# Optimization experiments

Measured on AMD Instinct MI355X. Metric: run time of the kernel, lower is better.

Reference implementation:

```python
import jax, jax.numpy as jnp
import numpy as np

EPS = 1e-8
MIN_VAL = -1e7  # min_val for masked_max padding


def _cos(v1, v2, axis=-1):
    # torch.F.cosine_similarity: dot / (max(||v1||,eps) * max(||v2||,eps))
    n1 = jnp.maximum(jnp.linalg.norm(v1, axis=axis), EPS)
    n2 = jnp.maximum(jnp.linalg.norm(v2, axis=axis), EPS)
    return jnp.sum(v1 * v2, axis=axis) / (n1 * n2)


def _mpm(v1, v2, w):
    # v1: (B,S,H), v2: (B,S,H) or (B,1,H), w: (P,H)
    mv_one = _cos(v1, v2)[..., None]                 # (B,S,1)
    v1w = w[None, None] * v1[:, :, None, :]          # (B,S,P,H)
    v2w = w[None, None] * v2[:, :, None, :]          # (B,S or 1,P,H)
    mv_many = _cos(v1w, v2w)                          # (B,S,P)
    return mv_one, mv_many


def _mpm_pairwise(v1, v2, w):
    # v1: (B,S1,H), v2: (B,S2,H), w: (P,H) -> (B,S1,S2,P)
    v1w = w[None, :, None, :] * v1[:, None]          # (B,P,S1,H)
    v2w = w[None, :, None, :] * v2[:, None]          # (B,P,S2,H)
    n1 = jnp.linalg.norm(v1w, axis=3)[..., None]     # (B,P,S1,1)
    n2 = jnp.linalg.norm(v2w, axis=3)[..., None]     # (B,P,S2,1)
    mul = jnp.einsum('bpih,bpjh->bpij', v1w, v2w)    # (B,P,S1,S2)
    norm = jnp.maximum(n1 * jnp.swapaxes(n2, 2, 3), EPS)
    return jnp.transpose(mul / norm, (0, 2, 3, 1))


def _masked_max(v, m, axis, keepdims=False):
    return jnp.max(v + (1.0 - m) * MIN_VAL, axis=axis, keepdims=keepdims)


def _masked_mean(v, m, axis, keepdims=False):
    s = jnp.sum(v, axis=axis, keepdims=keepdims)
    c = jnp.sum(m, axis=axis, keepdims=keepdims)
    return s / jnp.maximum(c, EPS)


def _bimpm(context_p, mask_p, context_h, mask_h, w_full, w_maxpool, w_att, w_maxatt):
    mp = mask_p.astype(context_p.dtype)              # (B,S1)
    mh = mask_h.astype(context_h.dtype)              # (B,S2)
    len_p = jnp.sum(mask_p, axis=1)
    len_h = jnp.sum(mask_h, axis=1)
    cp = context_p * mp[..., None]
    ch = context_h * mh[..., None]

    # pairwise cosine similarity (B,S1,S2)
    cos = _cos(cp[:, :, None, :], ch[:, None, :, :])
    cos_max_p = _masked_max(cos, mh[:, None, :], 2, True)
    cos_mean_p = _masked_mean(cos, mh[:, None, :], 2, True)
    cosT = jnp.swapaxes(cos, 1, 2)
    cos_max_h = _masked_max(cosT, mp[:, None, :], 2, True)
    cos_mean_h = _masked_mean(cosT, mp[:, None, :], 2, True)
    mv_p = [cos_max_p, cos_mean_p]
    mv_h = [cos_max_h, cos_mean_h]

    # full match (is_forward=True -> use last valid token)
    B, _, H = cp.shape
    idx_p = jnp.maximum(len_p - 1, 0)[:, None, None]
    idx_h = jnp.maximum(len_h - 1, 0)[:, None, None]
    last_p = jnp.take_along_axis(cp, jnp.broadcast_to(idx_p, (B, 1, H)), axis=1)
    last_h = jnp.take_along_axis(ch, jnp.broadcast_to(idx_h, (B, 1, H)), axis=1)
    o, m = _mpm(cp, last_h, w_full); mv_p += [o, m]
    o, m = _mpm(ch, last_p, w_full); mv_h += [o, m]

    # maxpool match over pairwise multi-perspective cosines (B,S1,S2,P)
    pw = _mpm_pairwise(cp, ch, w_maxpool)
    mv_p += [_masked_max(pw, mh[:, None, :, None], 2),
             _masked_mean(pw, mh[:, None, :, None], 2)]
    pwT = jnp.transpose(pw, (0, 2, 1, 3))
    mv_h += [_masked_max(pwT, mp[:, None, :, None], 2),
             _masked_mean(pwT, mp[:, None, :, None], 2)]

    # attentive match (mean-weighted by cosine attention)
    att = cos
    att_mean_h = jnp.einsum('bij,bjh->bih', att, ch) / jnp.maximum(
        jnp.sum(att, axis=2, keepdims=True), EPS)        # (B,S1,H)
    att_mean_p = jnp.einsum('bij,bih->bjh', att, cp) / jnp.maximum(
        jnp.swapaxes(jnp.sum(att, axis=1, keepdims=True), 1, 2), EPS)  # (B,S2,H)
    o, m = _mpm(cp, att_mean_h, w_att); mv_p += [o, m]
    o, m = _mpm(ch, att_mean_p, w_att); mv_h += [o, m]

    # max attentive match
    att_h_full = ch[:, None, :, :] * att[..., None]      # (B,S1,S2,H)
    att_max_h = _masked_max(att_h_full, mh[:, None, :, None], 2)  # (B,S1,H)
    att_p_full = cp[:, :, None, :] * att[..., None]      # (B,S1,S2,H)
    att_max_p = _masked_max(att_p_full, mp[:, :, None, None], 1)  # (B,S2,H)
    o, m = _mpm(cp, att_max_h, w_maxatt); mv_p += [o, m]
    o, m = _mpm(ch, att_max_p, w_maxatt); mv_h += [o, m]

    # (2, B, S, output_dim=105)
    return jnp.stack([jnp.concatenate(mv_p, axis=-1),
                      jnp.concatenate(mv_h, axis=-1)], axis=0)


def setup_inputs() -> dict:
    B, S1, S2, H, P = 8, 256, 256, 100, 20
    key = jax.random.key(0)
    ks = jax.random.split(key, 8)
    context_p = jax.random.normal(ks[0], (B, S1, H), jnp.float32)
    context_h = jax.random.normal(ks[1], (B, S2, H), jnp.float32)
    len_p = jax.random.randint(ks[2], (B,), S1 // 2, S1 + 1)
    len_h = jax.random.randint(ks[3], (B,), S2 // 2, S2 + 1)
    mask_p = (jnp.arange(S1)[None, :] < len_p[:, None]).astype(jnp.int32)
    mask_h = (jnp.arange(S2)[None, :] < len_h[:, None]).astype(jnp.int32)
    # four matching weights (share_weight_between_directions=True), torch.rand -> U[0,1)
    w_full = jax.random.uniform(ks[4], (P, H), jnp.float32)
    w_maxpool = jax.random.uniform(ks[5], (P, H), jnp.float32)
    w_att = jax.random.uniform(ks[6], (P, H), jnp.float32)
    w_maxatt = jax.random.uniform(ks[7], (P, H), jnp.float32)
    return {"context_p": context_p, "mask_p": mask_p, "context_h": context_h,
            "mask_h": mask_h, "w_full": w_full, "w_maxpool": w_maxpool,
            "w_att": w_att, "w_maxatt": w_maxatt}


def reference(context_p, mask_p, context_h, mask_h, w_full, w_maxpool, w_att, w_maxatt):
    return _bimpm(context_p, mask_p, context_h, mask_h, w_full, w_maxpool, w_att, w_maxatt)
```

## Files before the change

kernel.cpp:

```cpp
#include <hip/hip_runtime.h>

#define Bq 8
#define Sq 256
#define Hq 100
#define Pq 20
#define PPq 21
#define Fq 105
#define EPSq 1e-8f
#define NEGB -1e30f
#define IMG (128 * 136)

typedef short bf16x8 __attribute__((ext_vector_type(8)));
typedef float f32x4 __attribute__((ext_vector_type(4)));

__device__ __forceinline__ unsigned fkey(float f) {
    unsigned b = __float_as_uint(f);
    return (b & 0x80000000u) ? ~b : (b | 0x80000000u);
}
__device__ __forceinline__ float funkey(unsigned k) {
    return __uint_as_float((k & 0x80000000u) ? (k ^ 0x80000000u) : ~k);
}
__device__ __forceinline__ unsigned short bf16rn(float f) {
    unsigned u = __float_as_uint(f);
    unsigned r = u + 0x7FFFu + ((u >> 16) & 1u);
    return (unsigned short)(r >> 16);
}
__device__ __forceinline__ unsigned mulpack(unsigned pair, float w0, float w1) {
    float f0 = __uint_as_float(pair << 16);
    float f1 = __uint_as_float(pair & 0xFFFF0000u);
    f0 *= w0; f1 *= w1;
    return ((unsigned)bf16rn(f0)) | (((unsigned)bf16rn(f1)) << 16);
}

__global__ __launch_bounds__(256) void k_prep(
    const float* __restrict__ ctx_p, const int* __restrict__ mask_p,
    const float* __restrict__ ctx_h, const int* __restrict__ mask_h,
    const float* __restrict__ w_mp,
    float* __restrict__ vm, float* __restrict__ vmT,
    float* __restrict__ mf, float* __restrict__ wn,
    unsigned short* __restrict__ a16,
    float* __restrict__ lens, int* __restrict__ lasts,
    unsigned* __restrict__ statinit) {
    __shared__ float tileT[Hq * 257];
    __shared__ float w2T[Hq * 20];
    __shared__ float smf[256];
    __shared__ int ired[256];
    int side = blockIdx.x >> 3;
    int b = blockIdx.x & 7;
    int t = threadIdx.x;

    for (int idx = blockIdx.x * 256 + t; idx < 4 * Bq * PPq * Sq; idx += 16 * 256)
        statinit[idx] = 0u;

    const float* ctx = side ? ctx_h : ctx_p;
    const int* mask = side ? mask_h : mask_p;
    int mi = mask[b * Sq + t];
    smf[t] = (float)mi;
    ired[t] = mi;
    for (int idx = t; idx < Pq * Hq; idx += 256) {
        int p = idx / Hq, h = idx - p * Hq;
        float w = w_mp[idx];
        w2T[h * 20 + p] = w * w;
    }
    __syncthreads();
    for (int o = 128; o; o >>= 1) {
        if (t < o) ired[t] += ired[t + o];
        __syncthreads();
    }
    if (t == 0) {
        int l = ired[0];
        lens[side * Bq + b] = (float)l;
        lasts[side * Bq + b] = l > 0 ? l - 1 : 0;
    }

    unsigned short* abase = a16 + (size_t)(side * Bq + b) * 2 * IMG;
    {
        ushort4 z = {0, 0, 0, 0};
        for (int idx = t; idx < 2304; idx += 256) {
            int half = idx >= 1152;
            int rr = idx - half * 1152;
            int r = rr / 9, c = rr - r * 9;
            *(ushort4*)(abase + half * IMG + r * 136 + 100 + c * 4) = z;
        }
    }

    const float4* src = (const float4*)(ctx + (size_t)b * Sq * Hq);
    float4* vmo = (float4*)(vm + ((size_t)side * Bq + b) * Sq * Hq);
#pragma unroll
    for (int q = 0; q < 25; q++) {
        int F = t + 256 * q;
        int s = F / 25;
        int c = F - s * 25;
        float m = smf[s];
        float4 v4 = src[F];
        v4.x *= m; v4.y *= m; v4.z *= m; v4.w *= m;
        vmo[F] = v4;
        int h0 = c * 4;
        tileT[(h0 + 0) * 257 + s] = v4.x;
        tileT[(h0 + 1) * 257 + s] = v4.y;
        tileT[(h0 + 2) * 257 + s] = v4.z;
        tileT[(h0 + 3) * 257 + s] = v4.w;
        ushort4 o;
        o.x = bf16rn(v4.x); o.y = bf16rn(v4.y); o.z = bf16rn(v4.z); o.w = bf16rn(v4.w);
        *(ushort4*)(abase + (s >> 7) * IMG + (s & 127) * 136 + c * 4) = o;
    }
    __syncthreads();

    int s = t;
    float acc[PPq];
#pragma unroll
    for (int p = 0; p < PPq; p++) acc[p] = 0.f;
    float* vmTo = vmT + ((size_t)side * Bq + b) * Hq * Sq;
#pragma unroll 4
    for (int h = 0; h < Hq; h++) {
        float v = tileT[h * 257 + s];
        vmTo[h * Sq + s] = v;
        float e = v * v;
        acc[Pq] += e;
        const float4* wrow = (const float4*)(w2T + h * 20);
#pragma unroll
        for (int pq = 0; pq < 5; pq++) {
            float4 w4 = wrow[pq];
            acc[pq * 4 + 0] += w4.x * e;
            acc[pq * 4 + 1] += w4.y * e;
            acc[pq * 4 + 2] += w4.z * e;
            acc[pq * 4 + 3] += w4.w * e;
        }
    }
    float* wout = wn + ((size_t)side * Bq + b) * PPq * Sq;
#pragma unroll
    for (int p = 0; p < PPq; p++)
        wout[p * Sq + s] = 1.f / fmaxf(sqrtf(acc[p]), EPSq);
    mf[(size_t)side * Bq * Sq + b * Sq + s] = smf[s];
}

__global__ __launch_bounds__(256) void k_pw(
    const unsigned short* __restrict__ a16,
    const float* __restrict__ vmT,
    const float* __restrict__ wn, const float* __restrict__ mf,
    const float* __restrict__ w_mp, const float* __restrict__ lens,
    float* __restrict__ out, float* __restrict__ cosm, float* __restrict__ cosT,
    unsigned* __restrict__ rowmax, float* __restrict__ rowsum,
    unsigned* __restrict__ colmax, float* __restrict__ colsum) {
    __shared__ unsigned short As[IMG];
    __shared__ unsigned short Bs[IMG];
    __shared__ float w2s[144];
    int blk = blockIdx.x;
    int t = threadIdx.x;

    if (blk >= 64) {
        int mblk = blk - 64;
        int b = mblk / 80;
        int rem = mblk - b * 80;
        int p = rem >> 2;
        int ih = (rem >> 1) & 1, jh = rem & 1;
        int i0 = ih * 128, j0 = jh * 128;

        if (t < 144) {
            float w = (t < Hq) ? w_mp[p * Hq + t] : 0.f;
            w2s[t] = w * w;
        }
        __syncthreads();

        {
            const uint4* sa = (const uint4*)(a16 + (size_t)(b * 2 + ih) * IMG);
            uint4* dA = (uint4*)As;
#pragma unroll
            for (int q = 0; q < 9; q++) {
                int idx = t + 256 * q;
                if (idx < 2176) dA[idx] = sa[idx];
            }
        }
        {
            const uint4* sb = (const uint4*)(a16 + (size_t)((Bq + b) * 2 + jh) * IMG);
            uint4* dB = (uint4*)Bs;
#pragma unroll
            for (int q = 0; q < 9; q++) {
                int idx = t + 256 * q;
                if (idx < 2176) {
                    int cc = idx - (idx / 17) * 17;
                    int hb = cc * 8;
                    uint4 ch = sb[idx];
                    float4 wA = *(const float4*)(w2s + hb);
                    float4 wB = *(const float4*)(w2s + hb + 4);
                    uint4 o;
                    o.x = mulpack(ch.x, wA.x, wA.y);
                    o.y = mulpack(ch.y, wA.z, wA.w);
                    o.z = mulpack(ch.z, wB.x, wB.y);
                    o.w = mulpack(ch.w, wB.z, wB.w);
                    dB[idx] = o;
                }
            }
        }
        __syncthreads();

        int lane = t & 63;
        int wv = t >> 6;
        int wr = wv & 1, wc = wv >> 1;
        int lm = lane & 15, lq = lane >> 4;

        f32x4 acc[4][4];
#pragma unroll
        for (int tm = 0; tm < 4; tm++)
#pragma unroll
            for (int tn = 0; tn < 4; tn++) acc[tm][tn] = 0.f;

#pragma unroll
        for (int ks = 0; ks < 4; ks++) {
            bf16x8 af[4], bfr[4];
#pragma unroll
            for (int tm = 0; tm < 4; tm++)
                af[tm] = *(const bf16x8*)&As[(wr * 64 + tm * 16 + lm) * 136 + ks * 32 + lq * 8];
#pragma unroll
            for (int tn = 0; tn < 4; tn++)
                bfr[tn] = *(const bf16x8*)&Bs[(wc * 64 + tn * 16 + lm) * 136 + ks * 32 + lq * 8];
#pragma unroll
            for (int tm = 0; tm < 4; tm++)
#pragma unroll
                for (int tn = 0; tn < 4; tn++)
                    acc[tm][tn] = __builtin_amdgcn_mfma_f32_16x16x32_bf16(af[tm], bfr[tn], acc[tm][tn], 0, 0, 0);
        }

        const float* wn0 = wn + ((size_t)b * PPq + p) * Sq;
        const float* wn1 = wn + ((size_t)(Bq + b) * PPq + p) * Sq;
        const float* mfp = mf + b * Sq;
        const float* mfh = mf + (size_t)Bq * Sq + b * Sq;
        size_t base = ((size_t)b * PPq + p) * Sq;
        float rn2v[4], mzh[4];
#pragma unroll
        for (int tn = 0; tn < 4; tn++) {
            int jj = j0 + wc * 64 + tn * 16 + lm;
            rn2v[tn] = wn1[jj];
            mzh[tn] = mfh[jj] > 0.5f ? 0.f : NEGB;
        }
        float cmax[4] = {NEGB, NEGB, NEGB, NEGB};
        float csum[4] = {0.f, 0.f, 0.f, 0.f};
#pragma unroll
        for (int tm = 0; tm < 4; tm++) {
            int ibase = i0 + wr * 64 + tm * 16 + lq * 4;
            float rn1v[4], mzp[4];
#pragma unroll
            for (int r2 = 0; r2 < 4; r2++) {
                rn1v[r2] = wn0[ibase + r2];
                mzp[r2] = mfp[ibase + r2] > 0.5f ? 0.f : NEGB;
            }
            float rmax[4] = {NEGB, NEGB, NEGB, NEGB};
            float rsum[4] = {0.f, 0.f, 0.f, 0.f};
#pragma unroll
            for (int tn = 0; tn < 4; tn++)
#pragma unroll
                for (int r2 = 0; r2 < 4; r2++) {
                    float v = acc[tm][tn][r2] * rn1v[r2] * rn2v[tn];
                    rmax[r2] = fmaxf(rmax[r2], v + mzh[tn]);
                    rsum[r2] += v;
                    cmax[tn] = fmaxf(cmax[tn], v + mzp[r2]);
                    csum[tn] += v;
                }
#pragma unroll
            for (int r2 = 0; r2 < 4; r2++)
#pragma unroll
                for (int o = 1; o < 16; o <<= 1) {
                    rmax[r2] = fmaxf(rmax[r2], __shfl_xor(rmax[r2], o, 64));
                    rsum[r2] += __shfl_xor(rsum[r2], o, 64);
                }
            if (lm == 0) {
#pragma unroll
                for (int r2 = 0; r2 < 4; r2++) {
                    atomicMax(rowmax + base + ibase + r2, fkey(rmax[r2]));
                    atomicAdd(rowsum + base + ibase + r2, rsum[r2]);
                }
            }
        }
#pragma unroll
        for (int tn = 0; tn < 4; tn++) {
#pragma unroll
            for (int o = 16; o < 64; o <<= 1) {
                cmax[tn] = fmaxf(cmax[tn], __shfl_xor(cmax[tn], o, 64));
                csum[tn] += __shfl_xor(csum[tn], o, 64);
            }
        }
        if (lq == 0) {
#pragma unroll
            for (int tn = 0; tn < 4; tn++) {
                int jj = j0 + wc * 64 + tn * 16 + lm;
                atomicMax(colmax + base + jj, fkey(cmax[tn]));
                atomicAdd(colsum + base + jj, csum[tn]);
            }
        }
        return;
    }

    float (*cbmax)[Sq] = (float (*)[Sq])As;
    float (*cbsum)[Sq] = (float (*)[Sq])(As + 8192);
    int b = blk >> 3, it = blk & 7;
    int lane = t & 63;
    int wid = __builtin_amdgcn_readfirstlane(t >> 6);
    int i0 = it * 32 + wid * 8;

    const float* abase2 = vmT + (size_t)b * Hq * Sq;
    const float* bbase2 = vmT + (size_t)(Bq + b) * Hq * Sq;

    float4 acc[8];
#pragma unroll
    for (int k = 0; k < 8; k++) acc[k] = make_float4(0.f, 0.f, 0.f, 0.f);

#pragma unroll 4
    for (int h = 0; h < Hq; h++) {
        float4 bq = ((const float4*)(bbase2 + h * Sq))[lane];
        const float4* ap = (const float4*)(abase2 + h * Sq + i0);
        float4 a0 = ap[0], a1 = ap[1];
        float av[8] = {a0.x, a0.y, a0.z, a0.w, a1.x, a1.y, a1.z, a1.w};
#pragma unroll
        for (int k = 0; k < 8; k++) {
            acc[k].x += av[k] * bq.x; acc[k].y += av[k] * bq.y;
            acc[k].z += av[k] * bq.z; acc[k].w += av[k] * bq.w;
        }
    }

    const float* wn0 = wn + ((size_t)b * PPq + Pq) * Sq;
    const float* wn1 = wn + ((size_t)(Bq + b) * PPq + Pq) * Sq;
    float4 rn2 = ((const float4*)wn1)[lane];
    float4 mh4 = ((const float4*)(mf + (size_t)Bq * Sq + b * Sq))[lane];
    float invLh = 1.f / fmaxf(lens[Bq + b], EPSq);

    float cmax[4] = {NEGB, NEGB, NEGB, NEGB};
    float csum[4] = {0.f, 0.f, 0.f, 0.f};
#pragma unroll
    for (int k = 0; k < 8; k++) {
        float r1 = wn0[i0 + k];
        float4 v;
        v.x = acc[k].x * r1 * rn2.x;
        v.y = acc[k].y * r1 * rn2.y;
        v.z = acc[k].z * r1 * rn2.z;
        v.w = acc[k].w * r1 * rn2.w;
        float m0 = mh4.x > 0.5f ? v.x : NEGB;
        float m1 = mh4.y > 0.5f ? v.y : NEGB;
        float m2 = mh4.z > 0.5f ? v.z : NEGB;
        float m3 = mh4.w > 0.5f ? v.w : NEGB;
        float rmax = fmaxf(fmaxf(m0, m1), fmaxf(m2, m3));
        float rs = v.x + v.y + v.z + v.w;
        for (int o = 32; o; o >>= 1) {
            rmax = fmaxf(rmax, __shfl_xor(rmax, o, 64));
            rs += __shfl_xor(rs, o, 64);
        }
        if (lane == 0) {
            float* orow = out + ((size_t)(b * Sq + i0 + k)) * Fq;
            orow[0] = rmax;
            orow[1] = rs * invLh;
        }
        float mi = mf[b * Sq + i0 + k];
        if (mi > 0.5f) {
            cmax[0] = fmaxf(cmax[0], v.x); cmax[1] = fmaxf(cmax[1], v.y);
            cmax[2] = fmaxf(cmax[2], v.z); cmax[3] = fmaxf(cmax[3], v.w);
        }
        csum[0] += v.x; csum[1] += v.y; csum[2] += v.z; csum[3] += v.w;
        ((float4*)(cosm + (size_t)(b * Sq + i0 + k) * Sq))[lane] = v;
        int jb = 4 * lane;
        cosT[((size_t)b * Sq + jb + 0) * Sq + i0 + k] = v.x;
        cosT[((size_t)b * Sq + jb + 1) * Sq + i0 + k] = v.y;
        cosT[((size_t)b * Sq + jb + 2) * Sq + i0 + k] = v.z;
        cosT[((size_t)b * Sq + jb + 3) * Sq + i0 + k] = v.w;
    }
    ((float4*)&cbmax[wid][0])[lane] = make_float4(cmax[0], cmax[1], cmax[2], cmax[3]);
    ((float4*)&cbsum[wid][0])[lane] = make_float4(csum[0], csum[1], csum[2], csum[3]);
    __syncthreads();
    {
        int j = t;
        float mx = fmaxf(fmaxf(cbmax[0][j], cbmax[1][j]), fmaxf(cbmax[2][j], cbmax[3][j]));
        float sm = cbsum[0][j] + cbsum[1][j] + cbsum[2][j] + cbsum[3][j];
        size_t cidx = ((size_t)b * PPq + Pq) * Sq + j;
        atomicMax(colmax + cidx, fkey(mx));
        atomicAdd(colsum + cidx, sm);
    }
}

__global__ __launch_bounds__(256) void k_att(
    const float* __restrict__ vm, const float* __restrict__ mf,
    const float* __restrict__ cosm, const float* __restrict__ cosT,
    const unsigned* __restrict__ rowmax, const float* __restrict__ rowsum,
    const unsigned* __restrict__ colmax, const float* __restrict__ colsum,
    const float* __restrict__ lens,
    float* __restrict__ out,
    float* __restrict__ attvT) {
    __shared__ float L[Sq * 8];
    __shared__ float bm[Sq];
    int blk = blockIdx.x;
    int t = threadIdx.x;

    if (blk < Bq * PPq) {
        int bcf = blk / PPq, pcf = blk - bcf * PPq;
        float mx = funkey(colmax[(size_t)blk * Sq + t]);
        float sm = colsum[(size_t)blk * Sq + t];
        float invLp = 1.f / fmaxf(lens[bcf], EPSq);
        float* orow = out + (size_t)Bq * Sq * Fq + (size_t)(bcf * Sq + t) * Fq;
        if (pcf < Pq) { orow[23 + pcf] = mx; orow[43 + pcf] = sm * invLp; }
        else { orow[0] = mx; orow[1] = sm * invLp; }
    } else if (blk < 2 * Bq * PPq) {
        int rf = blk - Bq * PPq;
        int bcf = rf / PPq, pcf = rf - bcf * PPq;
        if (pcf < Pq) {
            float mx = funkey(rowmax[(size_t)(bcf * PPq + pcf) * Sq + t]);
            float sm = rowsum[(size_t)(bcf * PPq + pcf) * Sq + t];
            float invLh = 1.f / fmaxf(lens[Bq + bcf], EPSq);
            float* orow = out + (size_t)(bcf * Sq + t) * Fq;
            orow[23 + pcf] = mx; orow[43 + pcf] = sm * invLh;
        }
    }

    int d = blk >> 8;
    int rem = blk & 255;
    int b = rem >> 5, rt = rem & 31;
    int r0 = rt * 8;
    int h = t & 127, rh = t >> 7;

    const float* src = (d ? cosm : cosT) + (size_t)b * Sq * Sq;
#pragma unroll
    for (int q = 0; q < 2; q++) {
        int F = t + 256 * q;
        int k = F >> 1, c = F & 1;
        float4 v4 = *(const float4*)(src + (size_t)k * Sq + r0 + c * 4);
        *(float4*)(L + k * 8 + c * 4) = v4;
    }
    bm[t] = (mf[(size_t)(1 - d) * Bq * Sq + b * Sq + t] > 0.5f) ? 0.f : NEGB;
    __syncthreads();

    const float* vB = vm + (size_t)(1 - d) * Bq * Sq * Hq + (size_t)b * Sq * Hq + h;
    bool hv = (h < Hq);
    float am[4] = {0.f, 0.f, 0.f, 0.f};
    float ax[4] = {NEGB, NEGB, NEGB, NEGB};
#pragma unroll 16
    for (int k = 0; k < Sq; k++) {
        float v = hv ? vB[(size_t)k * Hq] : 0.f;
        float4 w = *(const float4*)(L + k * 8 + rh * 4);
        float bk = bm[k];
        float p0 = w.x * v, p1 = w.y * v, p2 = w.z * v, p3 = w.w * v;
        am[0] += p0; am[1] += p1; am[2] += p2; am[3] += p3;
        ax[0] = fmaxf(ax[0], p0 + bk); ax[1] = fmaxf(ax[1], p1 + bk);
        ax[2] = fmaxf(ax[2], p2 + bk); ax[3] = fmaxf(ax[3], p3 + bk);
    }
    if (hv) {
        int rb = r0 + rh * 4;
        float4 m4 = make_float4(am[0], am[1], am[2], am[3]);
        float4 x4 = make_float4(ax[0], ax[1], ax[2], ax[3]);
        *(float4*)(attvT + (((size_t)(d * 2 + 0) * Bq + b) * Hq + h) * Sq + rb) = m4;
        *(float4*)(attvT + (((size_t)(d * 2 + 1) * Bq + b) * Hq + h) * Sq + rb) = x4;
    }
}

__global__ __launch_bounds__(128) void k_final(
    const float* __restrict__ vm, const float* __restrict__ vmT,
    const int* __restrict__ lasts, const float* __restrict__ attvT,
    const float* __restrict__ w_full, const float* __restrict__ w_att,
    const float* __restrict__ w_maxatt,
    float* __restrict__ out) {
    __shared__ float w2s[Hq * 2];
    __shared__ float v2u[Hq];
    int blk = blockIdx.x;
    int m = blk / 320;
    int rem = blk - m * 320;
    int dir = rem / 160; rem -= dir * 160;
    int b = rem / 20;    rem -= b * 20;
    int sc = rem / 10;
    int ps = rem - sc * 10;
    int t = threadIdx.x;
    const float* W = (m == 0) ? w_full : (m == 1) ? w_att : w_maxatt;
    for (int idx = t; idx < 2 * Hq; idx += 128) {
        int pp = idx / Hq, h = idx - pp * Hq;
        float w = W[(ps * 2 + pp) * Hq + h];
        w2s[h * 2 + pp] = w * w;
    }
    if (m == 0 && t < Hq) {
        int lastO = dir ? lasts[b] : lasts[Bq + b];
        v2u[t] = vm[(size_t)(1 - dir) * Bq * Sq * Hq + ((size_t)b * Sq + lastO) * Hq + t];
    }
    __syncthreads();

    int s = sc * 128 + t;
    const float* v1T = vmT + (size_t)(dir * Bq + b) * Hq * Sq + s;
    const float* v2T = attvT + ((size_t)(dir * 2 + (m == 2 ? 1 : 0)) * Bq + b) * Hq * Sq + s;

    float d0 = 0.f, a0 = 0.f, b0 = 0.f;
    float d1 = 0.f, a1 = 0.f, b1 = 0.f;
    float pd = 0.f, p1 = 0.f, p2 = 0.f;
#pragma unroll 4
    for (int h = 0; h < Hq; h++) {
        float v1 = v1T[h * Sq];
        float v2 = (m == 0) ? v2u[h] : v2T[h * Sq];
        float e1 = v1 * v2, e2 = v1 * v1, e3 = v2 * v2;
        float w0 = w2s[h * 2], w1 = w2s[h * 2 + 1];
        d0 += w0 * e1; a0 += w0 * e2; b0 += w0 * e3;
        d1 += w1 * e1; a1 += w1 * e2; b1 += w1 * e3;
        if (ps == 0) { pd += e1; p1 += e2; p2 += e3; }
    }
    int fbase = (m == 0) ? 2 : (m == 1) ? 63 : 84;
    float* orow = out + (size_t)dir * Bq * Sq * Fq + ((size_t)b * Sq + s) * Fq;
    if (ps == 0)
        orow[fbase] = pd / (fmaxf(sqrtf(p1), EPSq) * fmaxf(sqrtf(p2), EPSq));
    orow[fbase + 1 + ps * 2]     = d0 / (fmaxf(sqrtf(a0), EPSq) * fmaxf(sqrtf(b0), EPSq));
    orow[fbase + 1 + ps * 2 + 1] = d1 / (fmaxf(sqrtf(a1), EPSq) * fmaxf(sqrtf(b1), EPSq));
}

extern "C" void kernel_launch(void* const* d_in, const int* in_sizes, int n_in,
                              void* d_out, int out_size, void* d_ws, size_t ws_size,
                              hipStream_t stream) {
    (void)in_sizes; (void)n_in; (void)out_size; (void)ws_size;
    const float* ctx_p    = (const float*)d_in[0];
    const int*   mask_p   = (const int*)d_in[1];
    const float* ctx_h    = (const float*)d_in[2];
    const int*   mask_h   = (const int*)d_in[3];
    const float* w_full   = (const float*)d_in[4];
    const float* w_maxpool= (const float*)d_in[5];
    const float* w_att    = (const float*)d_in[6];
    const float* w_maxatt = (const float*)d_in[7];
    float* out = (float*)d_out;
    float* ws = (float*)d_ws;

    const size_t BSH = (size_t)Bq * Sq * Hq;
    const size_t BS  = (size_t)Bq * Sq;
    const size_t BSS = (size_t)Bq * Sq * Sq;
    const size_t BPS = (size_t)Bq * PPq * Sq;

    float* vm     = ws;               ws += 2 * BSH;
    float* vmT    = ws;               ws += 2 * BSH;
    unsigned short* a16 = (unsigned short*)ws;  ws += 2 * Bq * IMG / 2 * 2;
    float* mf     = ws;               ws += 2 * BS;
    float* wn     = ws;               ws += 2 * BPS;
    float* cosm   = ws;               ws += BSS;
    float* cosT   = ws;               ws += BSS;
    unsigned* rowmax = (unsigned*)ws; ws += BPS;
    float* rowsum = ws;               ws += BPS;
    unsigned* colmax = (unsigned*)ws; ws += BPS;
    float* colsum = ws;               ws += BPS;
    float* attvT  = ws;               ws += 4 * BSH;
    float* lens   = ws;               ws += 16;
    int*   lasts  = (int*)ws;         ws += 16;

    k_prep<<<16, 256, 0, stream>>>(ctx_p, mask_p, ctx_h, mask_h, w_maxpool,
                                   vm, vmT, mf, wn, a16, lens, lasts, rowmax);
    k_pw<<<704, 256, 0, stream>>>(a16, vmT, wn, mf, w_maxpool, lens,
                                  out, cosm, cosT, rowmax, rowsum, colmax, colsum);
    k_att<<<512, 256, 0, stream>>>(vm, mf, cosm, cosT, rowmax, rowsum, colmax, colsum,
                                   lens, out, attvT);
    k_final<<<960, 128, 0, stream>>>(vm, vmT, lasts, attvT, w_full, w_att, w_maxatt, out);
}
```

Before: 150.1 us.

## Split prep across sequence quarters and split attention reduction over K halves

```diff
diff --git a/kernel.cpp b/kernel.cpp
--- a/kernel.cpp
+++ b/kernel.cpp
@@ -41,80 +41,87 @@
     unsigned short* __restrict__ a16,
     float* __restrict__ lens, int* __restrict__ lasts,
     unsigned* __restrict__ statinit) {
-    __shared__ float tileT[Hq * 257];
+    __shared__ float tileT[Hq * 65];
     __shared__ float w2T[Hq * 20];
-    __shared__ float smf[256];
+    __shared__ float redp[PPq * 4 * 64];
+    __shared__ float smf[64];
     __shared__ int ired[256];
-    int side = blockIdx.x >> 3;
-    int b = blockIdx.x & 7;
+    int blk = blockIdx.x;
+    int side = blk >> 5;
+    int b = (blk >> 2) & 7;
+    int sq = blk & 3;
+    int s0 = sq * 64;
     int t = threadIdx.x;
 
-    for (int idx = blockIdx.x * 256 + t; idx < 4 * Bq * PPq * Sq; idx += 16 * 256)
+    for (int idx = blk * 256 + t; idx < 4 * Bq * PPq * Sq; idx += 64 * 256)
         statinit[idx] = 0u;
 
     const float* ctx = side ? ctx_h : ctx_p;
     const int* mask = side ? mask_h : mask_p;
-    int mi = mask[b * Sq + t];
-    smf[t] = (float)mi;
-    ired[t] = mi;
+    ired[t] = mask[b * Sq + t];
+    if (t < 64) smf[t] = (float)mask[b * Sq + s0 + t];
     for (int idx = t; idx < Pq * Hq; idx += 256) {
         int p = idx / Hq, h = idx - p * Hq;
         float w = w_mp[idx];
         w2T[h * 20 + p] = w * w;
     }
     __syncthreads();
-    for (int o = 128; o; o >>= 1) {
-        if (t < o) ired[t] += ired[t + o];
-        __syncthreads();
-    }
-    if (t == 0) {
-        int l = ired[0];
-        lens[side * Bq + b] = (float)l;
-        lasts[side * Bq + b] = l > 0 ? l - 1 : 0;
+    if (sq == 0) {
+        for (int o = 128; o; o >>= 1) {
+            if (t < o) ired[t] += ired[t + o];
+            __syncthreads();
+        }
+        if (t == 0) {
+            int l = ired[0];
+            lens[side * Bq + b] = (float)l;
+            lasts[side * Bq + b] = l > 0 ? l - 1 : 0;
+        }
     }
 
     unsigned short* abase = a16 + (size_t)(side * Bq + b) * 2 * IMG;
     {
         ushort4 z = {0, 0, 0, 0};
-        for (int idx = t; idx < 2304; idx += 256) {
-            int half = idx >= 1152;
-            int rr = idx - half * 1152;
-            int r = rr / 9, c = rr - r * 9;
-            *(ushort4*)(abase + half * IMG + r * 136 + 100 + c * 4) = z;
-        }
-    }
-
-    const float4* src = (const float4*)(ctx + (size_t)b * Sq * Hq);
-    float4* vmo = (float4*)(vm + ((size_t)side * Bq + b) * Sq * Hq);
-#pragma unroll
-    for (int q = 0; q < 25; q++) {
+        for (int idx = t; idx < 576; idx += 256) {
+            int r = idx / 9, c = idx - r * 9;
+            int g = s0 + r;
+            *(ushort4*)(abase + (g >> 7) * IMG + (g & 127) * 136 + 100 + c * 4) = z;
+        }
+    }
+
+    const float4* src = (const float4*)(ctx + ((size_t)b * Sq + s0) * Hq);
+    float4* vmo = (float4*)(vm + ((size_t)side * Bq + b) * Sq * Hq + (size_t)s0 * Hq);
+#pragma unroll
+    for (int q = 0; q < 7; q++) {
         int F = t + 256 * q;
-        int s = F / 25;
-        int c = F - s * 25;
-        float m = smf[s];
-        float4 v4 = src[F];
-        v4.x *= m; v4.y *= m; v4.z *= m; v4.w *= m;
-        vmo[F] = v4;
-        int h0 = c * 4;
-        tileT[(h0 + 0) * 257 + s] = v4.x;
-        tileT[(h0 + 1) * 257 + s] = v4.y;
-        tileT[(h0 + 2) * 257 + s] = v4.z;
-        tileT[(h0 + 3) * 257 + s] = v4.w;
-        ushort4 o;
-        o.x = bf16rn(v4.x); o.y = bf16rn(v4.y); o.z = bf16rn(v4.z); o.w = bf16rn(v4.w);
-        *(ushort4*)(abase + (s >> 7) * IMG + (s & 127) * 136 + c * 4) = o;
-    }
-    __syncthreads();
-
-    int s = t;
+        if (F < 1600) {
+            int s = F / 25, c = F - s * 25;
+            float m = smf[s];
+            float4 v4 = src[F];
+            v4.x *= m; v4.y *= m; v4.z *= m; v4.w *= m;
+            vmo[F] = v4;
+            int h0 = c * 4;
+            tileT[(h0 + 0) * 65 + s] = v4.x;
+            tileT[(h0 + 1) * 65 + s] = v4.y;
+            tileT[(h0 + 2) * 65 + s] = v4.z;
+            tileT[(h0 + 3) * 65 + s] = v4.w;
+            int g = s0 + s;
+            ushort4 o;
+            o.x = bf16rn(v4.x); o.y = bf16rn(v4.y); o.z = bf16rn(v4.z); o.w = bf16rn(v4.w);
+            *(ushort4*)(abase + (g >> 7) * IMG + (g & 127) * 136 + c * 4) = o;
+        }
+    }
+    __syncthreads();
+
+    int sl = t & 63, hq = t >> 6;
     float acc[PPq];
 #pragma unroll
     for (int p = 0; p < PPq; p++) acc[p] = 0.f;
-    float* vmTo = vmT + ((size_t)side * Bq + b) * Hq * Sq;
-#pragma unroll 4
-    for (int h = 0; h < Hq; h++) {
-        float v = tileT[h * 257 + s];
-        vmTo[h * Sq + s] = v;
+    float* vmTo = vmT + ((size_t)side * Bq + b) * Hq * Sq + s0;
+    int hbeg = hq * 25;
+#pragma unroll 5
+    for (int h = hbeg; h < hbeg + 25; h++) {
+        float v = tileT[h * 65 + sl];
+        vmTo[(size_t)h * Sq + sl] = v;
         float e = v * v;
         acc[Pq] += e;
         const float4* wrow = (const float4*)(w2T + h * 20);
@@ -127,11 +134,19 @@
             acc[pq * 4 + 3] += w4.w * e;
         }
     }
-    float* wout = wn + ((size_t)side * Bq + b) * PPq * Sq;
 #pragma unroll
     for (int p = 0; p < PPq; p++)
-        wout[p * Sq + s] = 1.f / fmaxf(sqrtf(acc[p]), EPSq);
-    mf[(size_t)side * Bq * Sq + b * Sq + s] = smf[s];
+        redp[(p * 4 + hq) * 64 + sl] = acc[p];
+    __syncthreads();
+
+    float* wout = wn + ((size_t)side * Bq + b) * PPq * Sq + s0;
+    for (int idx = t; idx < PPq * 64; idx += 256) {
+        int p = idx >> 6, s2 = idx & 63;
+        float ssum = redp[(p * 4 + 0) * 64 + s2] + redp[(p * 4 + 1) * 64 + s2] +
+                     redp[(p * 4 + 2) * 64 + s2] + redp[(p * 4 + 3) * 64 + s2];
+        wout[p * Sq + s2] = 1.f / fmaxf(sqrtf(ssum), EPSq);
+    }
+    if (t < 64) mf[(size_t)side * Bq * Sq + b * Sq + s0 + t] = smf[t];
 }
 
 __global__ __launch_bounds__(256) void k_pw(
@@ -374,7 +389,7 @@
     }
 }
 
-__global__ __launch_bounds__(256) void k_att(
+__global__ __launch_bounds__(512) void k_att(
     const float* __restrict__ vm, const float* __restrict__ mf,
     const float* __restrict__ cosm, const float* __restrict__ cosT,
     const unsigned* __restrict__ rowmax, const float* __restrict__ rowsum,
@@ -384,52 +399,56 @@
     float* __restrict__ attvT) {
     __shared__ float L[Sq * 8];
     __shared__ float bm[Sq];
+    __shared__ float pam[2][4][256];
+    __shared__ float pax[2][4][256];
     int blk = blockIdx.x;
     int t = threadIdx.x;
 
-    if (blk < Bq * PPq) {
-        int bcf = blk / PPq, pcf = blk - bcf * PPq;
-        float mx = funkey(colmax[(size_t)blk * Sq + t]);
-        float sm = colsum[(size_t)blk * Sq + t];
-        float invLp = 1.f / fmaxf(lens[bcf], EPSq);
-        float* orow = out + (size_t)Bq * Sq * Fq + (size_t)(bcf * Sq + t) * Fq;
-        if (pcf < Pq) { orow[23 + pcf] = mx; orow[43 + pcf] = sm * invLp; }
-        else { orow[0] = mx; orow[1] = sm * invLp; }
-    } else if (blk < 2 * Bq * PPq) {
-        int rf = blk - Bq * PPq;
-        int bcf = rf / PPq, pcf = rf - bcf * PPq;
-        if (pcf < Pq) {
-            float mx = funkey(rowmax[(size_t)(bcf * PPq + pcf) * Sq + t]);
-            float sm = rowsum[(size_t)(bcf * PPq + pcf) * Sq + t];
-            float invLh = 1.f / fmaxf(lens[Bq + bcf], EPSq);
-            float* orow = out + (size_t)(bcf * Sq + t) * Fq;
-            orow[23 + pcf] = mx; orow[43 + pcf] = sm * invLh;
-        }
+    if (t < 256) {
+        if (blk < Bq * PPq) {
+            int bcf = blk / PPq, pcf = blk - bcf * PPq;
+            float mx = funkey(colmax[(size_t)blk * Sq + t]);
+            float sm = colsum[(size_t)blk * Sq + t];
+            float invLp = 1.f / fmaxf(lens[bcf], EPSq);
+            float* orow = out + (size_t)Bq * Sq * Fq + (size_t)(bcf * Sq + t) * Fq;
+            if (pcf < Pq) { orow[23 + pcf] = mx; orow[43 + pcf] = sm * invLp; }
+            else { orow[0] = mx; orow[1] = sm * invLp; }
+        } else if (blk < 2 * Bq * PPq) {
+            int rf = blk - Bq * PPq;
+            int bcf = rf / PPq, pcf = rf - bcf * PPq;
+            if (pcf < Pq) {
+                float mx = funkey(rowmax[(size_t)(bcf * PPq + pcf) * Sq + t]);
+                float sm = rowsum[(size_t)(bcf * PPq + pcf) * Sq + t];
+                float invLh = 1.f / fmaxf(lens[Bq + bcf], EPSq);
+                float* orow = out + (size_t)(bcf * Sq + t) * Fq;
+                orow[23 + pcf] = mx; orow[43 + pcf] = sm * invLh;
+            }
+        }
+        bm[t] = (mf[(size_t)(1 - (blk >> 8)) * Bq * Sq + ((blk & 255) >> 5) * Sq + t] > 0.5f) ? 0.f : NEGB;
     }
 
     int d = blk >> 8;
     int rem = blk & 255;
     int b = rem >> 5, rt = rem & 31;
     int r0 = rt * 8;
-    int h = t & 127, rh = t >> 7;
+    int h = t & 127, rh = (t >> 7) & 1, kh = t >> 8;
 
     const float* src = (d ? cosm : cosT) + (size_t)b * Sq * Sq;
-#pragma unroll
-    for (int q = 0; q < 2; q++) {
-        int F = t + 256 * q;
-        int k = F >> 1, c = F & 1;
+    {
+        int k = t >> 1, c = t & 1;
         float4 v4 = *(const float4*)(src + (size_t)k * Sq + r0 + c * 4);
         *(float4*)(L + k * 8 + c * 4) = v4;
     }
-    bm[t] = (mf[(size_t)(1 - d) * Bq * Sq + b * Sq + t] > 0.5f) ? 0.f : NEGB;
     __syncthreads();
 
     const float* vB = vm + (size_t)(1 - d) * Bq * Sq * Hq + (size_t)b * Sq * Hq + h;
     bool hv = (h < Hq);
     float am[4] = {0.f, 0.f, 0.f, 0.f};
     float ax[4] = {NEGB, NEGB, NEGB, NEGB};
+    int k0 = kh * 128;
 #pragma unroll 16
-    for (int k = 0; k < Sq; k++) {
+    for (int kk = 0; kk < 128; kk++) {
+        int k = k0 + kk;
         float v = hv ? vB[(size_t)k * Hq] : 0.f;
         float4 w = *(const float4*)(L + k * 8 + rh * 4);
         float bk = bm[k];
@@ -438,10 +457,17 @@
         ax[0] = fmaxf(ax[0], p0 + bk); ax[1] = fmaxf(ax[1], p1 + bk);
         ax[2] = fmaxf(ax[2], p2 + bk); ax[3] = fmaxf(ax[3], p3 + bk);
     }
-    if (hv) {
+    int hr = t & 255;
+#pragma unroll
+    for (int r = 0; r < 4; r++) { pam[kh][r][hr] = am[r]; pax[kh][r][hr] = ax[r]; }
+    __syncthreads();
+    if (t < 256 && hv) {
         int rb = r0 + rh * 4;
-        float4 m4 = make_float4(am[0], am[1], am[2], am[3]);
-        float4 x4 = make_float4(ax[0], ax[1], ax[2], ax[3]);
+        float4 m4, x4;
+        m4.x = pam[0][0][t] + pam[1][0][t]; x4.x = fmaxf(pax[0][0][t], pax[1][0][t]);
+        m4.y = pam[0][1][t] + pam[1][1][t]; x4.y = fmaxf(pax[0][1][t], pax[1][1][t]);
+        m4.z = pam[0][2][t] + pam[1][2][t]; x4.z = fmaxf(pax[0][2][t], pax[1][2][t]);
+        m4.w = pam[0][3][t] + pam[1][3][t]; x4.w = fmaxf(pax[0][3][t], pax[1][3][t]);
         *(float4*)(attvT + (((size_t)(d * 2 + 0) * Bq + b) * Hq + h) * Sq + rb) = m4;
         *(float4*)(attvT + (((size_t)(d * 2 + 1) * Bq + b) * Hq + h) * Sq + rb) = x4;
     }
@@ -535,11 +561,11 @@
     float* lens   = ws;               ws += 16;
     int*   lasts  = (int*)ws;         ws += 16;
 
-    k_prep<<<16, 256, 0, stream>>>(ctx_p, mask_p, ctx_h, mask_h, w_maxpool,
+    k_prep<<<64, 256, 0, stream>>>(ctx_p, mask_p, ctx_h, mask_h, w_maxpool,
                                    vm, vmT, mf, wn, a16, lens, lasts, rowmax);
     k_pw<<<704, 256, 0, stream>>>(a16, vmT, wn, mf, w_maxpool, lens,
                                   out, cosm, cosT, rowmax, rowsum, colmax, colsum);
-    k_att<<<512, 256, 0, stream>>>(vm, mf, cosm, cosT, rowmax, rowsum, colmax, colsum,
+    k_att<<<512, 512, 0, stream>>>(vm, mf, cosm, cosT, rowmax, rowsum, colmax, colsum,
                                    lens, out, attvT);
     k_final<<<960, 128, 0, stream>>>(vm, vmT, lasts, attvT, w_full, w_att, w_maxatt, out);
 }
```

After: 135.5 us. 9.7% less time.
